# Performance work log

Measured on AMD Instinct MI355X. Metric: run time of the kernel, lower is better.

The kernel has to match this reference:

```python
import jax, jax.numpy as jnp
import numpy as np
from jax import lax

B, C, H, W = 8, 1024, 64, 48
A = 9  # anchors per location

def _conv(x, w, b, pad):
    y = lax.conv_general_dilated(x, w, (1, 1), pad,
                                 dimension_numbers=('NCHW', 'OIHW', 'NCHW'))
    return y + b[None, :, None, None]

def setup_inputs() -> dict:
    key = jax.random.key(0)
    ks = jax.random.split(key, 12)
    base_feat = jax.random.normal(ks[0], (B, C, H, W), dtype=jnp.float32)
    W_conv = jax.random.normal(ks[1], (512, C, 3, 3), dtype=jnp.float32) * 0.01
    b_conv = jnp.zeros((512,), jnp.float32)
    W_cls = jax.random.normal(ks[2], (18, 512, 1, 1), dtype=jnp.float32) * 0.01
    b_cls = jnp.zeros((18,), jnp.float32)
    W_bbox = jax.random.normal(ks[3], (36, 512, 1, 1), dtype=jnp.float32) * 0.01
    b_bbox = jnp.zeros((36,), jnp.float32)
    # anchor-target-layer outputs (data-dependent assignment) provided as inputs
    rpn_label = (jax.random.randint(ks[4], (B, A * H * W), 0, 3) - 1).astype(jnp.int32)  # {-1,0,1}
    rpn_bbox_targets = jax.random.normal(ks[5], (B, 36, H, W), dtype=jnp.float32) * 0.1
    rpn_bbox_inside_weights = (jax.random.uniform(ks[6], (B, 36, H, W)) < 0.25).astype(jnp.float32)
    rpn_bbox_outside_weights = jax.random.uniform(ks[7], (B, 36, H, W), dtype=jnp.float32) * 0.01
    return {"base_feat": base_feat, "W_conv": W_conv, "b_conv": b_conv,
            "W_cls": W_cls, "b_cls": b_cls, "W_bbox": W_bbox, "b_bbox": b_bbox,
            "rpn_label": rpn_label, "rpn_bbox_targets": rpn_bbox_targets,
            "rpn_bbox_inside_weights": rpn_bbox_inside_weights,
            "rpn_bbox_outside_weights": rpn_bbox_outside_weights}

def reference(base_feat, W_conv, b_conv, W_cls, b_cls, W_bbox, b_bbox,
              rpn_label, rpn_bbox_targets, rpn_bbox_inside_weights,
              rpn_bbox_outside_weights):
    # RPN head: 3x3 conv + relu, then 1x1 cls / bbox heads
    rpn_conv1 = jax.nn.relu(_conv(base_feat, W_conv, b_conv, ((1, 1), (1, 1))))
    cls_score = _conv(rpn_conv1, W_cls, b_cls, ((0, 0), (0, 0)))   # [B,18,H,W]
    bbox_pred = _conv(rpn_conv1, W_bbox, b_bbox, ((0, 0), (0, 0)))  # [B,36,H,W]
    # reshape to [B,2,A*H,W], softmax over the 2-way fg/bg axis, reshape back
    score_rs = cls_score.reshape(B, 2, A * H, W)
    prob_rs = jax.nn.softmax(score_rs, axis=1)
    rpn_cls_prob = prob_rs.reshape(B, 18, H, W)
    # classification loss: permute(0,2,3,1).view(-1,2), keep labels != -1
    logits = score_rs.transpose(0, 2, 3, 1).reshape(-1, 2)
    label = rpn_label.reshape(-1)
    valid = (label != -1).astype(logits.dtype)
    logp = jax.nn.log_softmax(logits, axis=-1)
    lbl = jnp.clip(label, 0, 1)
    nll = -jnp.take_along_axis(logp, lbl[:, None].astype(jnp.int32), axis=1)[:, 0]
    rpn_loss_cls = jnp.sum(nll * valid) / jnp.maximum(jnp.sum(valid), 1.0)
    # smooth-L1 box loss, sigma=3, summed over dims [1,2,3], mean over batch
    sigma2 = 9.0
    in_diff = rpn_bbox_inside_weights * (bbox_pred - rpn_bbox_targets)
    abs_d = jnp.abs(in_diff)
    sign = lax.stop_gradient((abs_d < 1.0 / sigma2).astype(abs_d.dtype))
    in_loss = in_diff * in_diff * (sigma2 / 2.0) * sign + (abs_d - 0.5 / sigma2) * (1.0 - sign)
    rpn_loss_box = jnp.mean(jnp.sum(rpn_bbox_outside_weights * in_loss, axis=(1, 2, 3)))
    return rpn_cls_prob, bbox_pred, rpn_loss_cls, rpn_loss_box
```

## Files before the change

kernel.cpp:

```cpp
#include <hip/hip_runtime.h>
#include <stdint.h>

#define B_    8
#define CIN   1024
#define H_    64
#define W_    48
#define OC    512
#define HW    3072
#define NPOS  24576
#define K9    9216
#define HP    66
#define WP    50

typedef __attribute__((ext_vector_type(8))) __bf16 bf16x8;
typedef __attribute__((ext_vector_type(4))) float  float4_t;
typedef __attribute__((ext_vector_type(4))) unsigned short ushort4_t;
typedef __attribute__((ext_vector_type(8))) int int8v;
typedef __attribute__((ext_vector_type(4))) int int4v;

__device__ __forceinline__ unsigned short f2bf(float x) {
  union { float f; unsigned u; } v; v.f = x;
  unsigned r = v.u + 0x7FFFu + ((v.u >> 16) & 1u);
  return (unsigned short)(r >> 16);
}

__device__ __forceinline__ unsigned int pack4_fp8(float a, float b, float c, float d) {
  int w = __builtin_amdgcn_cvt_pk_fp8_f32(a, b, 0, false);
  w = __builtin_amdgcn_cvt_pk_fp8_f32(c, d, w, true);
  return (unsigned int)w;
}

__device__ __forceinline__ void async16(const void* g, void* l) {
  __builtin_amdgcn_global_load_lds(
      (const __attribute__((address_space(1))) unsigned int*)g,
      (__attribute__((address_space(3))) unsigned int*)l, 16, 0, 0);
}

__device__ __forceinline__ float wave_sum(float v) {
  for (int o = 32; o > 0; o >>= 1) v += __shfl_down(v, o, 64);
  return v;
}

__global__ void prep_fused(const float* __restrict__ x, const float* __restrict__ Wc,
                           const float* __restrict__ Wcls, const float* __restrict__ Wbb,
                           unsigned char* __restrict__ xt, unsigned char* __restrict__ Wa,
                           unsigned short* __restrict__ Wh, float* __restrict__ accbuf) {
  __shared__ float smem[9216];
  int bid = blockIdx.x, t = threadIdx.x;
  if (bid < 4096) {
    int cx = bid & 7, h = (bid >> 3) & 63, b = bid >> 9;
    float* tile = smem;
    const float* src = x + ((long)(b * CIN + cx * 128) * H_ + h) * W_;
    for (int it = 0; it < 6; ++it) {
      int e = it * 256 + t;
      int cl = e / 12, w4 = e % 12;
      float4_t v = *(const float4_t*)&src[(long)cl * HW + w4 * 4];
      int base = cl * 49 + w4 * 4;
      tile[base] = v.x; tile[base + 1] = v.y; tile[base + 2] = v.z; tile[base + 3] = v.w;
    }
    __syncthreads();
    unsigned char* dst = xt + ((long)(b * HP + h + 1) * WP + 1) * CIN + cx * 128;
    for (int it = 0; it < 6; ++it) {
      int e = it * 256 + t;
      int w = e >> 5, g = e & 31;
      float v0 = tile[(g * 4 + 0) * 49 + w] * 16.f;
      float v1 = tile[(g * 4 + 1) * 49 + w] * 16.f;
      float v2 = tile[(g * 4 + 2) * 49 + w] * 16.f;
      float v3 = tile[(g * 4 + 3) * 49 + w] * 16.f;
      *(unsigned int*)&dst[(long)w * CIN + g * 4] = pack4_fp8(v0, v1, v2, v3);
    }
  } else if (bid < 4608) {
    int o = bid - 4096;
    float* lw = smem;
    const float* src = Wc + (long)o * K9;
    for (int i = 0; i < 9; ++i)
      *(float4_t*)&lw[i * 1024 + t * 4] = *(const float4_t*)&src[i * 1024 + t * 4];
    __syncthreads();
    unsigned char* dst = Wa + (long)o * K9;
    int c = t * 4;
    for (int off = 0; off < 9; ++off) {
      float v0 = lw[(c + 0) * 9 + off] * 512.f;
      float v1 = lw[(c + 1) * 9 + off] * 512.f;
      float v2 = lw[(c + 2) * 9 + off] * 512.f;
      float v3 = lw[(c + 3) * 9 + off] * 512.f;
      *(unsigned int*)&dst[off * 1024 + c] = pack4_fp8(v0, v1, v2, v3);
    }
  } else if (bid < 4640) {
    int e = (bid - 4608) * 1024 + t * 4;
    int m = e >> 9, c = e & 511;
    float v0 = 0.f, v1 = 0.f, v2 = 0.f, v3 = 0.f;
    if (m < 18) {
      const float* s = Wcls + m * 512 + c;
      v0 = s[0]; v1 = s[1]; v2 = s[2]; v3 = s[3];
    } else if (m < 54) {
      const float* s = Wbb + (m - 18) * 512 + c;
      v0 = s[0]; v1 = s[1]; v2 = s[2]; v3 = s[3];
    }
    ushort4_t pk; pk.x = f2bf(v0); pk.y = f2bf(v1); pk.z = f2bf(v2); pk.w = f2bf(v3);
    *(ushort4_t*)&Wh[e] = pk;
    if (bid == 4608 && t < 4) accbuf[t] = 0.f;
  } else {
    int bid2 = bid - 4640;
    int b = bid2 / 66, h = bid2 % 66;
    unsigned char* base = xt + (long)(b * 66 + h) * 50 * 1024;
    int4v z = {};
    if (h == 0 || h == 65) {
      for (int i = t; i < 3200; i += 256) *(int4v*)(base + (long)i * 16) = z;
    } else if (t < 128) {
      int which = t >> 6, off = t & 63;
      *(int4v*)(base + (long)which * 49 * 1024 + (long)off * 16) = z;
    }
  }
}

#define BKF 128
__global__ __launch_bounds__(256, 2)
void conv_gemm(const unsigned char* __restrict__ Wa, const unsigned char* __restrict__ xt,
               const float* __restrict__ bias, unsigned short* __restrict__ conv1) {
  __shared__ unsigned char As[128 * BKF];
  __shared__ unsigned char Bs[128 * BKF];
  int t = threadIdx.x;
  int lane = t & 63, wv = t >> 6;
  int m0 = blockIdx.y * 128;
  int n0 = blockIdx.x * 128;
  const unsigned char* aSrc[4];
  const unsigned char* bSrc[4];
  for (int s = 0; s < 4; ++s) {
    int c = s * 256 + t;
    int r = c >> 3;
    int q = (c & 7) ^ (r & 7);
    aSrc[s] = Wa + (long)(m0 + r) * K9 + q * 16;
    int n = n0 + r; int b = n / HW; int rem = n % HW; int h = rem / W_; int w = rem % W_;
    bSrc[s] = xt + ((long)(b * HP + h) * WP + w) * CIN + q * 16;
  }
  float4_t acc[4][4] = {};
  int wm = wv >> 1, wn = wv & 1;
  int quad = lane >> 4, col = lane & 15;
  for (int kt = 0; kt < 72; ++kt) {
    int off = kt >> 3;
    int dy = off / 3, dx = off % 3;
    long boff = (long)(dy * WP + dx) * CIN + (kt & 7) * 128;
    long aoff = (long)kt * 128;
    __syncthreads();
    for (int s = 0; s < 4; ++s)
      async16(aSrc[s] + aoff, &As[s * 4096 + wv * 1024]);
    for (int s = 0; s < 4; ++s)
      async16(bSrc[s] + boff, &Bs[s * 4096 + wv * 1024]);
    __syncthreads();
    int8v af[4], bfr[4];
    for (int i = 0; i < 4; ++i) {
      int r = wm * 64 + i * 16 + col;
      int rb = r * 128, x7 = r & 7;
      int4v lo = *(const int4v*)&As[rb + (((quad * 2 + 0) ^ x7) << 4)];
      int4v hi = *(const int4v*)&As[rb + (((quad * 2 + 1) ^ x7) << 4)];
      af[i] = (int8v){lo.x, lo.y, lo.z, lo.w, hi.x, hi.y, hi.z, hi.w};
    }
    for (int j = 0; j < 4; ++j) {
      int r = wn * 64 + j * 16 + col;
      int rb = r * 128, x7 = r & 7;
      int4v lo = *(const int4v*)&Bs[rb + (((quad * 2 + 0) ^ x7) << 4)];
      int4v hi = *(const int4v*)&Bs[rb + (((quad * 2 + 1) ^ x7) << 4)];
      bfr[j] = (int8v){lo.x, lo.y, lo.z, lo.w, hi.x, hi.y, hi.z, hi.w};
    }
    for (int i = 0; i < 4; ++i)
      for (int j = 0; j < 4; ++j)
        acc[i][j] = __builtin_amdgcn_mfma_scale_f32_16x16x128_f8f6f4(
            af[i], bfr[j], acc[i][j], 0, 0, 0, 0x76767676, 0, 0x7B7B7B7B);
  }
  for (int i = 0; i < 4; ++i) {
    int mb = m0 + wm * 64 + i * 16 + quad * 4;
    float b0 = bias[mb + 0], b1 = bias[mb + 1], b2 = bias[mb + 2], b3 = bias[mb + 3];
    for (int j = 0; j < 4; ++j) {
      int n = n0 + wn * 64 + j * 16 + col;
      ushort4_t pk;
      pk.x = f2bf(fmaxf(acc[i][j].x + b0, 0.f));
      pk.y = f2bf(fmaxf(acc[i][j].y + b1, 0.f));
      pk.z = f2bf(fmaxf(acc[i][j].z + b2, 0.f));
      pk.w = f2bf(fmaxf(acc[i][j].w + b3, 0.f));
      *(ushort4_t*)&conv1[(long)n * 512 + mb] = pk;
    }
  }
}

__global__ __launch_bounds__(256, 2)
void head_gemm(const unsigned short* __restrict__ Wh, const unsigned short* __restrict__ conv1,
               const float* __restrict__ b_cls, const float* __restrict__ b_bbox,
               float* __restrict__ cls_ws, float* __restrict__ out_bbox) {
  __shared__ unsigned short As[64 * 128];
  __shared__ unsigned short Bs[64 * 128];
  int t = threadIdx.x;
  int lane = t & 63, wv = t >> 6;
  int n0 = blockIdx.x * 64;
  int quad = lane >> 4, col = lane & 15;
  const unsigned short* aS[4];
  const unsigned short* bS[4];
  for (int p = 0; p < 4; ++p) {
    int c = p * 256 + t;
    int r = c >> 4;
    int q = (c & 15) ^ (r & 15);
    aS[p] = Wh + (long)r * 512 + q * 8;
    bS[p] = conv1 + (long)(n0 + r) * 512 + q * 8;
  }
  float4_t acc[4] = {};
  for (int kt = 0; kt < 4; ++kt) {
    long koff = (long)kt * 128;
    __syncthreads();
    for (int p = 0; p < 4; ++p) async16(aS[p] + koff, &As[p * 2048 + wv * 512]);
    for (int p = 0; p < 4; ++p) async16(bS[p] + koff, &Bs[p * 2048 + wv * 512]);
    __syncthreads();
    for (int ks = 0; ks < 4; ++ks) {
      int rn = wv * 16 + col;
      bf16x8 bfr = *(const bf16x8*)&Bs[rn * 128 + (((ks * 4 + quad) ^ (rn & 15)) << 3)];
      for (int i = 0; i < 4; ++i) {
        int r = i * 16 + col;
        bf16x8 af = *(const bf16x8*)&As[r * 128 + (((ks * 4 + quad) ^ (r & 15)) << 3)];
        acc[i] = __builtin_amdgcn_mfma_f32_16x16x32_bf16(af, bfr, acc[i], 0, 0, 0);
      }
    }
  }
  int n = n0 + wv * 16 + col;
  int b = n / HW; int rem = n % HW;
  for (int i = 0; i < 4; ++i) {
    for (int r = 0; r < 4; ++r) {
      int m = i * 16 + quad * 4 + r;
      float v = acc[i][r];
      if (m < 18) {
        cls_ws[(long)(b * 18 + m) * HW + rem] = v + b_cls[m];
      } else if (m < 54) {
        out_bbox[(long)(b * 36 + (m - 18)) * HW + rem] = v + b_bbox[m - 18];
      }
    }
  }
}

__global__ void loss_fused(const float* __restrict__ cls, const int* __restrict__ label,
                           float* __restrict__ prob,
                           const float* __restrict__ pred, const float* __restrict__ tgt,
                           const float* __restrict__ iw, const float* __restrict__ ow,
                           float* __restrict__ acc) {
  int lane = threadIdx.x & 63, wv = threadIdx.x >> 6;
  __shared__ float red[8];
  if (blockIdx.x < 864) {
    int idx = blockIdx.x * 256 + threadIdx.x;
    int b = idx / 27648; int r = idx % 27648;
    int a = r / HW; int r2 = r % HW;
    long i0 = (long)(b * 18 + a) * HW + r2;
    long i1 = i0 + (long)9 * HW;
    float x0 = cls[i0], x1 = cls[i1];
    float mx = fmaxf(x0, x1);
    float e0 = __expf(x0 - mx), e1 = __expf(x1 - mx);
    float s = e0 + e1;
    prob[i0] = e0 / s;
    prob[i1] = e1 / s;
    int lb = label[idx];
    float nll = 0.f, val = 0.f;
    if (lb != -1) {
      val = 1.f;
      float xl = (lb > 0) ? x1 : x0;
      nll = -(xl - mx - __logf(s));
    }
    nll = wave_sum(nll);
    val = wave_sum(val);
    if (lane == 0) { red[wv] = nll; red[4 + wv] = val; }
    __syncthreads();
    if (threadIdx.x == 0) {
      atomicAdd(&acc[0], red[0] + red[1] + red[2] + red[3]);
      atomicAdd(&acc[1], red[4] + red[5] + red[6] + red[7]);
    }
  } else {
    int bid = blockIdx.x - 864;
    float s = 0.f;
    const long total = (long)B_ * 36 * HW;
    for (long i = (long)bid * 256 + threadIdx.x; i < total; i += (long)1728 * 256) {
      float d = iw[i] * (pred[i] - tgt[i]);
      float ad = fabsf(d);
      float l = (ad < (1.f / 9.f)) ? d * d * 4.5f : ad - (1.f / 18.f);
      s += ow[i] * l;
    }
    s = wave_sum(s);
    if (lane == 0) red[wv] = s;
    __syncthreads();
    if (threadIdx.x == 0) atomicAdd(&acc[2], red[0] + red[1] + red[2] + red[3]);
  }
}

__global__ void finalize(const float* __restrict__ acc, float* __restrict__ out) {
  if (threadIdx.x == 0) {
    out[0] = acc[0] / fmaxf(acc[1], 1.f);
    out[1] = acc[2] / (float)B_;
  }
}

extern "C" void kernel_launch(void* const* d_in, const int* in_sizes, int n_in,
                              void* d_out, int out_size, void* d_ws, size_t ws_size,
                              hipStream_t stream) {
  const float* base_feat = (const float*)d_in[0];
  const float* W_conv    = (const float*)d_in[1];
  const float* b_conv    = (const float*)d_in[2];
  const float* W_cls     = (const float*)d_in[3];
  const float* b_cls     = (const float*)d_in[4];
  const float* W_bbox    = (const float*)d_in[5];
  const float* b_bbox    = (const float*)d_in[6];
  const int*   rpn_label = (const int*)d_in[7];
  const float* bb_tgt    = (const float*)d_in[8];
  const float* bb_iw     = (const float*)d_in[9];
  const float* bb_ow     = (const float*)d_in[10];

  float* out = (float*)d_out;
  float* out_cls_prob = out;
  float* out_bbox     = out + 442368;
  float* out_scalars  = out + 442368 + 884736;

  size_t off = 0;
  auto alloc = [&](size_t bytes) {
    void* p = (char*)d_ws + off;
    off = (off + bytes + 255) & ~(size_t)255;
    return p;
  };
  const size_t XT_BYTES = (size_t)B_ * HP * WP * CIN;
  unsigned char*  xt    = (unsigned char*)alloc(XT_BYTES);
  unsigned char*  Wa    = (unsigned char*)alloc((size_t)OC * K9);
  unsigned short* conv1 = (unsigned short*)alloc((size_t)NPOS * OC * 2);
  unsigned short* Wh    = (unsigned short*)alloc((size_t)64 * 512 * 2);
  float* cls_ws         = (float*)alloc((size_t)B_ * 18 * HW * 4);
  float* accbuf         = (float*)alloc(16);

  prep_fused<<<5168, 256, 0, stream>>>(base_feat, W_conv, W_cls, W_bbox, xt, Wa, Wh, accbuf);
  conv_gemm<<<dim3(192, 4), 256, 0, stream>>>(Wa, xt, b_conv, conv1);
  head_gemm<<<384, 256, 0, stream>>>(Wh, conv1, b_cls, b_bbox, cls_ws, out_bbox);
  loss_fused<<<2592, 256, 0, stream>>>(cls_ws, rpn_label, out_cls_prob,
                                       out_bbox, bb_tgt, bb_iw, bb_ow, accbuf);
  finalize<<<1, 64, 0, stream>>>(accbuf, out_scalars);
}
```

Baseline: 355.2 us.

## Double-buffer conv GEMM LDS tiles and fold finalize into loss kernel

The conv GEMM K-loop now uses two LDS buffers for the A and B tiles. It issues the async load for the next k-tile before computing on the current one, which removes one barrier per iteration and overlaps global-to-LDS traffic with MFMA work. LDS use doubles to 64KB per block, which may limit occupancy under launch_bounds(256,2). The finalize launch is removed: the last block to finish loss_fused, found with an atomic ticket counter, writes the scalar losses. This relies on acc[3] being zeroed by prep and on the fence and atomic-read ordering being correct.

Result: slower. 463.9 us (+30.6%).

```diff
diff --git a/kernel.cpp b/kernel.cpp
--- a/kernel.cpp
+++ b/kernel.cpp
@@ -117,8 +117,8 @@
 __global__ __launch_bounds__(256, 2)
 void conv_gemm(const unsigned char* __restrict__ Wa, const unsigned char* __restrict__ xt,
                const float* __restrict__ bias, unsigned short* __restrict__ conv1) {
-  __shared__ unsigned char As[128 * BKF];
-  __shared__ unsigned char Bs[128 * BKF];
+  __shared__ unsigned char As[2][128 * BKF];
+  __shared__ unsigned char Bs[2][128 * BKF];
   int t = threadIdx.x;
   int lane = t & 63, wv = t >> 6;
   int m0 = blockIdx.y * 128;
@@ -136,30 +136,36 @@
   float4_t acc[4][4] = {};
   int wm = wv >> 1, wn = wv & 1;
   int quad = lane >> 4, col = lane & 15;
-  for (int kt = 0; kt < 72; ++kt) {
+
+  auto stage = [&](int kt, int pb) {
     int off = kt >> 3;
     int dy = off / 3, dx = off % 3;
     long boff = (long)(dy * WP + dx) * CIN + (kt & 7) * 128;
     long aoff = (long)kt * 128;
-    __syncthreads();
     for (int s = 0; s < 4; ++s)
-      async16(aSrc[s] + aoff, &As[s * 4096 + wv * 1024]);
+      async16(aSrc[s] + aoff, &As[pb][s * 4096 + wv * 1024]);
     for (int s = 0; s < 4; ++s)
-      async16(bSrc[s] + boff, &Bs[s * 4096 + wv * 1024]);
-    __syncthreads();
+      async16(bSrc[s] + boff, &Bs[pb][s * 4096 + wv * 1024]);
+  };
+
+  stage(0, 0);
+  for (int kt = 0; kt < 72; ++kt) {
+    int pb = kt & 1;
+    __syncthreads();
+    if (kt < 71) stage(kt + 1, pb ^ 1);
     int8v af[4], bfr[4];
     for (int i = 0; i < 4; ++i) {
       int r = wm * 64 + i * 16 + col;
       int rb = r * 128, x7 = r & 7;
-      int4v lo = *(const int4v*)&As[rb + (((quad * 2 + 0) ^ x7) << 4)];
-      int4v hi = *(const int4v*)&As[rb + (((quad * 2 + 1) ^ x7) << 4)];
+      int4v lo = *(const int4v*)&As[pb][rb + (((quad * 2 + 0) ^ x7) << 4)];
+      int4v hi = *(const int4v*)&As[pb][rb + (((quad * 2 + 1) ^ x7) << 4)];
       af[i] = (int8v){lo.x, lo.y, lo.z, lo.w, hi.x, hi.y, hi.z, hi.w};
     }
     for (int j = 0; j < 4; ++j) {
       int r = wn * 64 + j * 16 + col;
       int rb = r * 128, x7 = r & 7;
-      int4v lo = *(const int4v*)&Bs[rb + (((quad * 2 + 0) ^ x7) << 4)];
-      int4v hi = *(const int4v*)&Bs[rb + (((quad * 2 + 1) ^ x7) << 4)];
+      int4v lo = *(const int4v*)&Bs[pb][rb + (((quad * 2 + 0) ^ x7) << 4)];
+      int4v hi = *(const int4v*)&Bs[pb][rb + (((quad * 2 + 1) ^ x7) << 4)];
       bfr[j] = (int8v){lo.x, lo.y, lo.z, lo.w, hi.x, hi.y, hi.z, hi.w};
     }
     for (int i = 0; i < 4; ++i)
@@ -237,7 +243,7 @@
                            float* __restrict__ prob,
                            const float* __restrict__ pred, const float* __restrict__ tgt,
                            const float* __restrict__ iw, const float* __restrict__ ow,
-                           float* __restrict__ acc) {
+                           float* __restrict__ acc, float* __restrict__ out_scalars) {
   int lane = threadIdx.x & 63, wv = threadIdx.x >> 6;
   __shared__ float red[8];
   if (blockIdx.x < 864) {
@@ -282,12 +288,16 @@
     __syncthreads();
     if (threadIdx.x == 0) atomicAdd(&acc[2], red[0] + red[1] + red[2] + red[3]);
   }
-}
-
-__global__ void finalize(const float* __restrict__ acc, float* __restrict__ out) {
   if (threadIdx.x == 0) {
-    out[0] = acc[0] / fmaxf(acc[1], 1.f);
-    out[1] = acc[2] / (float)B_;
+    __threadfence();
+    float tk = atomicAdd(&acc[3], 1.f);
+    if (tk == 2591.f) {
+      float c0 = atomicAdd(&acc[0], 0.f);
+      float c1 = atomicAdd(&acc[1], 0.f);
+      float c2 = atomicAdd(&acc[2], 0.f);
+      out_scalars[0] = c0 / fmaxf(c1, 1.f);
+      out_scalars[1] = c2 / (float)B_;
+    }
   }
 }
 
@@ -329,6 +339,5 @@
   conv_gemm<<<dim3(192, 4), 256, 0, stream>>>(Wa, xt, b_conv, conv1);
   head_gemm<<<384, 256, 0, stream>>>(Wh, conv1, b_cls, b_bbox, cls_ws, out_bbox);
   loss_fused<<<2592, 256, 0, stream>>>(cls_ws, rpn_label, out_cls_prob,
-                                       out_bbox, bb_tgt, bb_iw, bb_ow, accbuf);
-  finalize<<<1, 64, 0, stream>>>(accbuf, out_scalars);
-}
+                                       out_bbox, bb_tgt, bb_iw, bb_ow, accbuf, out_scalars);
+}
```

## Fuse 1x1 head GEMM into conv epilogue via atomic partial sums

Applied to the files above, without the earlier changes.

The conv GEMM epilogue now stages its bf16 ReLU tile in shared memory and multiplies it directly by the matching 128-channel slice of the head weights. Partial head outputs are accumulated with float atomics into a zeroed head_acc buffer, and the 4 M-blocks each contribute to every output. This removes the conv1 intermediate round-trip and the separate head_gemm launch. The finalize kernel is folded into loss_fused through a last-block counter, and the bbox output write plus bias add move into the loss kernel. In exchange it adds many global atomics, a larger zeroing pass, and strided gathers in the loss kernel.

After: 394.3 us. 1.11x slower.

```diff
diff --git a/kernel.cpp b/kernel.cpp
--- a/kernel.cpp
+++ b/kernel.cpp
@@ -44,7 +44,8 @@
 __global__ void prep_fused(const float* __restrict__ x, const float* __restrict__ Wc,
                            const float* __restrict__ Wcls, const float* __restrict__ Wbb,
                            unsigned char* __restrict__ xt, unsigned char* __restrict__ Wa,
-                           unsigned short* __restrict__ Wh, float* __restrict__ accbuf) {
+                           unsigned short* __restrict__ Wh, float* __restrict__ accbuf,
+                           float* __restrict__ head_acc) {
   __shared__ float smem[9216];
   int bid = blockIdx.x, t = threadIdx.x;
   if (bid < 4096) {
@@ -99,7 +100,7 @@
     ushort4_t pk; pk.x = f2bf(v0); pk.y = f2bf(v1); pk.z = f2bf(v2); pk.w = f2bf(v3);
     *(ushort4_t*)&Wh[e] = pk;
     if (bid == 4608 && t < 4) accbuf[t] = 0.f;
-  } else {
+  } else if (bid < 5168) {
     int bid2 = bid - 4640;
     int b = bid2 / 66, h = bid2 % 66;
     unsigned char* base = xt + (long)(b * 66 + h) * 50 * 1024;
@@ -110,15 +111,22 @@
       int which = t >> 6, off = t & 63;
       *(int4v*)(base + (long)which * 49 * 1024 + (long)off * 16) = z;
     }
+  } else {
+    long base = (long)(bid - 5168) * 4096 + t * 16;
+    float4_t z = {};
+    for (int i = 0; i < 4; ++i) *(float4_t*)&head_acc[base + i * 4] = z;
   }
 }
 
 #define BKF 128
 __global__ __launch_bounds__(256, 2)
 void conv_gemm(const unsigned char* __restrict__ Wa, const unsigned char* __restrict__ xt,
-               const float* __restrict__ bias, unsigned short* __restrict__ conv1) {
-  __shared__ unsigned char As[128 * BKF];
-  __shared__ unsigned char Bs[128 * BKF];
+               const float* __restrict__ bias, const unsigned short* __restrict__ Wh,
+               float* __restrict__ head_acc) {
+  __shared__ __align__(16) unsigned char sm[32768];
+  unsigned char* As = sm;
+  unsigned char* Bs = sm + 16384;
+  unsigned short* P = (unsigned short*)sm;
   int t = threadIdx.x;
   int lane = t & 63, wv = t >> 6;
   int m0 = blockIdx.y * 128;
@@ -167,91 +175,63 @@
         acc[i][j] = __builtin_amdgcn_mfma_scale_f32_16x16x128_f8f6f4(
             af[i], bfr[j], acc[i][j], 0, 0, 0, 0x76767676, 0, 0x7B7B7B7B);
   }
+  __syncthreads();
   for (int i = 0; i < 4; ++i) {
     int mb = m0 + wm * 64 + i * 16 + quad * 4;
+    int ml = wm * 64 + i * 16 + quad * 4;
     float b0 = bias[mb + 0], b1 = bias[mb + 1], b2 = bias[mb + 2], b3 = bias[mb + 3];
+    int chunk = ml >> 3, sub = ml & 7;
     for (int j = 0; j < 4; ++j) {
-      int n = n0 + wn * 64 + j * 16 + col;
+      int nl = wn * 64 + j * 16 + col;
       ushort4_t pk;
       pk.x = f2bf(fmaxf(acc[i][j].x + b0, 0.f));
       pk.y = f2bf(fmaxf(acc[i][j].y + b1, 0.f));
       pk.z = f2bf(fmaxf(acc[i][j].z + b2, 0.f));
       pk.w = f2bf(fmaxf(acc[i][j].w + b3, 0.f));
-      *(ushort4_t*)&conv1[(long)n * 512 + mb] = pk;
-    }
-  }
-}
-
-__global__ __launch_bounds__(256, 2)
-void head_gemm(const unsigned short* __restrict__ Wh, const unsigned short* __restrict__ conv1,
-               const float* __restrict__ b_cls, const float* __restrict__ b_bbox,
-               float* __restrict__ cls_ws, float* __restrict__ out_bbox) {
-  __shared__ unsigned short As[64 * 128];
-  __shared__ unsigned short Bs[64 * 128];
-  int t = threadIdx.x;
-  int lane = t & 63, wv = t >> 6;
-  int n0 = blockIdx.x * 64;
-  int quad = lane >> 4, col = lane & 15;
-  const unsigned short* aS[4];
-  const unsigned short* bS[4];
-  for (int p = 0; p < 4; ++p) {
-    int c = p * 256 + t;
-    int r = c >> 4;
-    int q = (c & 15) ^ (r & 15);
-    aS[p] = Wh + (long)r * 512 + q * 8;
-    bS[p] = conv1 + (long)(n0 + r) * 512 + q * 8;
-  }
-  float4_t acc[4] = {};
-  for (int kt = 0; kt < 4; ++kt) {
-    long koff = (long)kt * 128;
-    __syncthreads();
-    for (int p = 0; p < 4; ++p) async16(aS[p] + koff, &As[p * 2048 + wv * 512]);
-    for (int p = 0; p < 4; ++p) async16(bS[p] + koff, &Bs[p * 2048 + wv * 512]);
-    __syncthreads();
-    for (int ks = 0; ks < 4; ++ks) {
-      int rn = wv * 16 + col;
-      bf16x8 bfr = *(const bf16x8*)&Bs[rn * 128 + (((ks * 4 + quad) ^ (rn & 15)) << 3)];
-      for (int i = 0; i < 4; ++i) {
-        int r = i * 16 + col;
-        bf16x8 af = *(const bf16x8*)&As[r * 128 + (((ks * 4 + quad) ^ (r & 15)) << 3)];
-        acc[i] = __builtin_amdgcn_mfma_f32_16x16x32_bf16(af, bfr, acc[i], 0, 0, 0);
+      *(ushort4_t*)((unsigned char*)P + nl * 256 + (((chunk ^ (nl & 15)) << 4) + sub * 2)) = pk;
+    }
+  }
+  __syncthreads();
+  for (int mt = 0; mt < 4; ++mt) {
+    for (int nt = 0; nt < 2; ++nt) {
+      int nl = wv * 32 + nt * 16 + col;
+      float4_t acc2 = {};
+      for (int ks = 0; ks < 4; ++ks) {
+        bf16x8 af2 = *(const bf16x8*)&Wh[(mt * 16 + col) * 512 + m0 + ks * 32 + quad * 8];
+        int ch = ks * 4 + quad;
+        bf16x8 bf2 = *(const bf16x8*)((unsigned char*)P + nl * 256 + ((ch ^ (nl & 15)) << 4));
+        acc2 = __builtin_amdgcn_mfma_f32_16x16x32_bf16(af2, bf2, acc2, 0, 0, 0);
       }
-    }
-  }
-  int n = n0 + wv * 16 + col;
-  int b = n / HW; int rem = n % HW;
-  for (int i = 0; i < 4; ++i) {
-    for (int r = 0; r < 4; ++r) {
-      int m = i * 16 + quad * 4 + r;
-      float v = acc[i][r];
-      if (m < 18) {
-        cls_ws[(long)(b * 18 + m) * HW + rem] = v + b_cls[m];
-      } else if (m < 54) {
-        out_bbox[(long)(b * 36 + (m - 18)) * HW + rem] = v + b_bbox[m - 18];
+      int n = n0 + nl;
+      for (int r = 0; r < 4; ++r) {
+        int mh = mt * 16 + quad * 4 + r;
+        if (mh < 54) atomicAdd(&head_acc[(long)mh * NPOS + n], acc2[r]);
       }
     }
   }
 }
 
-__global__ void loss_fused(const float* __restrict__ cls, const int* __restrict__ label,
-                           float* __restrict__ prob,
-                           const float* __restrict__ pred, const float* __restrict__ tgt,
+__global__ void loss_fused(const float* __restrict__ head_acc, const int* __restrict__ label,
+                           const float* __restrict__ b_cls, const float* __restrict__ b_bbox,
+                           float* __restrict__ prob, float* __restrict__ out_bbox,
+                           const float* __restrict__ tgt,
                            const float* __restrict__ iw, const float* __restrict__ ow,
-                           float* __restrict__ acc) {
+                           float* __restrict__ acc, float* __restrict__ out_scalars) {
   int lane = threadIdx.x & 63, wv = threadIdx.x >> 6;
   __shared__ float red[8];
   if (blockIdx.x < 864) {
     int idx = blockIdx.x * 256 + threadIdx.x;
     int b = idx / 27648; int r = idx % 27648;
     int a = r / HW; int r2 = r % HW;
-    long i0 = (long)(b * 18 + a) * HW + r2;
-    long i1 = i0 + (long)9 * HW;
-    float x0 = cls[i0], x1 = cls[i1];
+    long nn = (long)b * HW + r2;
+    float x0 = head_acc[(long)a * NPOS + nn] + b_cls[a];
+    float x1 = head_acc[(long)(a + 9) * NPOS + nn] + b_cls[a + 9];
     float mx = fmaxf(x0, x1);
     float e0 = __expf(x0 - mx), e1 = __expf(x1 - mx);
     float s = e0 + e1;
+    long i0 = (long)(b * 18 + a) * HW + r2;
     prob[i0] = e0 / s;
-    prob[i1] = e1 / s;
+    prob[i0 + (long)9 * HW] = e1 / s;
     int lb = label[idx];
     float nll = 0.f, val = 0.f;
     if (lb != -1) {
@@ -272,7 +252,12 @@
     float s = 0.f;
     const long total = (long)B_ * 36 * HW;
     for (long i = (long)bid * 256 + threadIdx.x; i < total; i += (long)1728 * 256) {
-      float d = iw[i] * (pred[i] - tgt[i]);
+      int hw = (int)(i % HW);
+      int c = (int)((i / HW) % 36);
+      int b = (int)(i / (36 * HW));
+      float pv = head_acc[(long)(18 + c) * NPOS + (long)b * HW + hw] + b_bbox[c];
+      out_bbox[i] = pv;
+      float d = iw[i] * (pv - tgt[i]);
       float ad = fabsf(d);
       float l = (ad < (1.f / 9.f)) ? d * d * 4.5f : ad - (1.f / 18.f);
       s += ow[i] * l;
@@ -282,12 +267,16 @@
     __syncthreads();
     if (threadIdx.x == 0) atomicAdd(&acc[2], red[0] + red[1] + red[2] + red[3]);
   }
-}
-
-__global__ void finalize(const float* __restrict__ acc, float* __restrict__ out) {
   if (threadIdx.x == 0) {
-    out[0] = acc[0] / fmaxf(acc[1], 1.f);
-    out[1] = acc[2] / (float)B_;
+    __threadfence();
+    float tk = atomicAdd(&acc[3], 1.f);
+    if (tk == 2591.f) {
+      float c0 = atomicAdd(&acc[0], 0.f);
+      float c1 = atomicAdd(&acc[1], 0.f);
+      float c2 = atomicAdd(&acc[2], 0.f);
+      out_scalars[0] = c0 / fmaxf(c1, 1.f);
+      out_scalars[1] = c2 / (float)B_;
+    }
   }
 }
 
@@ -320,15 +309,14 @@
   const size_t XT_BYTES = (size_t)B_ * HP * WP * CIN;
   unsigned char*  xt    = (unsigned char*)alloc(XT_BYTES);
   unsigned char*  Wa    = (unsigned char*)alloc((size_t)OC * K9);
-  unsigned short* conv1 = (unsigned short*)alloc((size_t)NPOS * OC * 2);
   unsigned short* Wh    = (unsigned short*)alloc((size_t)64 * 512 * 2);
-  float* cls_ws         = (float*)alloc((size_t)B_ * 18 * HW * 4);
+  float* head_acc       = (float*)alloc((size_t)64 * NPOS * 4);
   float* accbuf         = (float*)alloc(16);
 
-  prep_fused<<<5168, 256, 0, stream>>>(base_feat, W_conv, W_cls, W_bbox, xt, Wa, Wh, accbuf);
-  conv_gemm<<<dim3(192, 4), 256, 0, stream>>>(Wa, xt, b_conv, conv1);
-  head_gemm<<<384, 256, 0, stream>>>(Wh, conv1, b_cls, b_bbox, cls_ws, out_bbox);
-  loss_fused<<<2592, 256, 0, stream>>>(cls_ws, rpn_label, out_cls_prob,
-                                       out_bbox, bb_tgt, bb_iw, bb_ow, accbuf);
-  finalize<<<1, 64, 0, stream>>>(accbuf, out_scalars);
-}
+  prep_fused<<<5552, 256, 0, stream>>>(base_feat, W_conv, W_cls, W_bbox, xt, Wa, Wh,
+                                       accbuf, head_acc);
+  conv_gemm<<<dim3(192, 4), 256, 0, stream>>>(Wa, xt, b_conv, Wh, head_acc);
+  loss_fused<<<2592, 256, 0, stream>>>(head_acc, rpn_label, b_cls, b_bbox,
+                                       out_cls_prob, out_bbox, bb_tgt, bb_iw, bb_ow,
+                                       accbuf, out_scalars);
+}
```
